# Kernel tuning notes

Measured on AMD Instinct MI355X. Metric: run time of the kernel, lower is better.

Reference implementation:

```python
import jax, jax.numpy as jnp
import numpy as np
import math

N_EMBD = 2048
N_HEAD = 16
RATIO_KV = 4
N_HEAD_KV = N_HEAD // RATIO_KV
HEAD_DIM = N_EMBD // N_HEAD


def alibi_slopes(n_heads):
    def pow2_slopes(n):
        start = 2 ** (-2 ** (-(math.log2(n) - 3)))
        return [start * start ** i for i in range(n)]
    if math.log2(n_heads).is_integer():
        return jnp.asarray(pow2_slopes(n_heads), dtype=jnp.float32)
    closest = 2 ** math.floor(math.log2(n_heads))
    base = pow2_slopes(closest)
    if n_heads <= 2 * closest:
        s = base + base[0::2]
    else:
        s = base + base[0::2] + base[1::2]
    return jnp.asarray(s[:n_heads], dtype=jnp.float32)


def setup_inputs() -> dict:
    key = jax.random.key(0)
    k0, k1, k2, k3, k4 = jax.random.split(key, 5)
    B, T = 4, 2048
    x = jax.random.normal(k0, (B, T, N_EMBD), dtype=jnp.float32)
    s = 0.02
    Wq = jax.random.normal(k1, (N_EMBD, N_EMBD), dtype=jnp.float32) * s
    Wk = jax.random.normal(k2, (N_EMBD, N_HEAD_KV * HEAD_DIM), dtype=jnp.float32) * s
    Wv = jax.random.normal(k3, (N_EMBD, N_HEAD_KV * HEAD_DIM), dtype=jnp.float32) * s
    Wo = jax.random.normal(k4, (N_EMBD, N_EMBD), dtype=jnp.float32) * s
    return {"x": x, "Wq": Wq, "Wk": Wk, "Wv": Wv, "Wo": Wo}


def reference(x, Wq, Wk, Wv, Wo):
    B, T, C = x.shape
    group = N_HEAD // N_HEAD_KV
    # projections (no bias, dropout=0 eval)
    q = (x @ Wq).reshape(B, T, N_HEAD, HEAD_DIM).transpose(0, 2, 1, 3)      # [B,H,T,D]
    k = (x @ Wk).reshape(B, T, N_HEAD_KV, HEAD_DIM).transpose(0, 2, 1, 3)   # [B,Hkv,T,D]
    v = (x @ Wv).reshape(B, T, N_HEAD_KV, HEAD_DIM).transpose(0, 2, 1, 3)
    # GQA repeat_interleave along head dim
    k = jnp.repeat(k, group, axis=1)  # [B,H,T,D]
    v = jnp.repeat(v, group, axis=1)
    scale = 1.0 / math.sqrt(HEAD_DIM)
    att = jnp.einsum('bhqd,bhkd->bhqk', q, k) * scale  # [B,H,T,T]
    # ALiBi bias: slopes[h] * (j - i), with torch's repeat_interleave-by-group
    slopes = alibi_slopes(N_HEAD)
    slopes = jnp.repeat(slopes, group)[:N_HEAD]  # matches repeat_interleave(dim=0)[:n_head]
    pos = jnp.arange(T)
    rel = pos[None, :] - pos[:, None]  # [T,T]
    bias = slopes[:, None, None] * rel.astype(jnp.float32)[None, :, :]  # [H,T,T]
    causal = jnp.triu(jnp.full((T, T), -jnp.inf, dtype=jnp.float32), k=1)
    att = att + bias[None] + causal[None, None]
    att = jax.nn.softmax(att.astype(jnp.float32), axis=-1).astype(q.dtype)
    y = jnp.einsum('bhqk,bhkd->bhqd', att, v)  # [B,H,T,D]
    y = y.transpose(0, 2, 1, 3).reshape(B, T, C)
    return y @ Wo
```

## Files before the change

### kernel.cpp

```cpp
#include <hip/hip_runtime.h>
#include <hip/hip_bf16.h>

#define T_SEQ 2048
#define NB 4
#define NE 2048
#define NH 16
#define NHKV 4
#define HD 128
#define KVD 512
#define MTOT 8192

typedef __attribute__((ext_vector_type(4))) float f32x4;
typedef __attribute__((ext_vector_type(16))) float f32x16;
typedef __attribute__((ext_vector_type(8))) __bf16 bf16x8;

__device__ __forceinline__ unsigned short f2bf(float f) {
  union { float f; unsigned int u; } x; x.f = f;
  unsigned int u = x.u;
  unsigned int r = (u + 0x7fffu + ((u >> 16) & 1u)) >> 16;
  return (unsigned short)r;
}

__device__ __forceinline__ unsigned cvtpk(float lo, float hi) {
  unsigned r;
  asm("v_cvt_pk_bf16_f32 %0, %1, %2" : "=v"(r) : "v"(lo), "v"(hi));
  return r;
}

__device__ __forceinline__ void plswap(unsigned &a, unsigned &b) {
  asm volatile("v_permlane32_swap_b32 %0, %1" : "+v"(a), "+v"(b));
}

typedef __attribute__((address_space(3))) unsigned int lds_uint;
typedef const __attribute__((address_space(1))) unsigned int glob_uint;

__device__ __forceinline__ void gload_lds16(const void* g, void* l) {
  __builtin_amdgcn_global_load_lds((glob_uint*)g, (lds_uint*)l, 16, 0, 0);
}

__global__ __launch_bounds__(256) void k_cast(const float* __restrict__ in,
                                              unsigned short* __restrict__ out, int n) {
  int i = (blockIdx.x * blockDim.x + threadIdx.x) * 8;
  if (i >= n) return;
  float4 a = *(const float4*)(in + i);
  float4 b = *(const float4*)(in + i + 4);
  union { unsigned short us[8]; uint4 v; } o;
  o.us[0] = f2bf(a.x); o.us[1] = f2bf(a.y); o.us[2] = f2bf(a.z); o.us[3] = f2bf(a.w);
  o.us[4] = f2bf(b.x); o.us[5] = f2bf(b.y); o.us[6] = f2bf(b.z); o.us[7] = f2bf(b.w);
  *(uint4*)(out + i) = o.v;
}

__global__ __launch_bounds__(256) void k_transpose_cast(const float* __restrict__ in,
                                                        unsigned short* __restrict__ out,
                                                        int K, int N) {
  __shared__ float tile[32][33];
  int n0 = blockIdx.x * 32, k0 = blockIdx.y * 32;
  int tx = threadIdx.x & 31, ty = threadIdx.x >> 5;
#pragma unroll
  for (int r = 0; r < 4; ++r)
    tile[ty + r * 8][tx] = in[(k0 + ty + r * 8) * N + n0 + tx];
  __syncthreads();
#pragma unroll
  for (int r = 0; r < 4; ++r)
    out[(n0 + ty + r * 8) * K + k0 + tx] = f2bf(tile[tx][ty + r * 8]);
}

template <int STORE_MODE>
__global__ __launch_bounds__(256) void k_gemm(const unsigned short* __restrict__ A,
                                              const unsigned short* __restrict__ Bt,
                                              void* __restrict__ C,
                                              int M, int N, int K) {
  __shared__ alignas(16) unsigned short lds[2][2][128 * 32];
  const int tid = threadIdx.x;
  const int w = tid >> 6, lane = tid & 63;
  const int lg = lane >> 4, ll = lane & 15;
  const int m0 = blockIdx.y * 128, n0 = blockIdx.x * 128;
  const int wr = (w >> 1) * 64, wc = (w & 1) * 64;

  f32x4 acc[4][4] = {};

  const int NT = K >> 5;
  int cur = 0;

  auto STAGE = [&](int buf, int t) {
    int k0 = t << 5;
#pragma unroll
    for (int is = 0; is < 2; ++is) {
      int chunk = is * 256 + tid;
      int r = chunk >> 2, c = chunk & 3;
      int sc = (c ^ ((r >> 1) & 3)) << 3;
      gload_lds16(A + (m0 + r) * K + k0 + sc, &lds[buf][0][(is * 256 + (w << 6)) * 8]);
      gload_lds16(Bt + (n0 + r) * K + k0 + sc, &lds[buf][1][(is * 256 + (w << 6)) * 8]);
    }
  };

  auto COMPUTE = [&](int buf) {
    const unsigned short* La = lds[buf][0];
    const unsigned short* Lb = lds[buf][1];
    bf16x8 af[4], bfr[4];
#pragma unroll
    for (int mf = 0; mf < 4; ++mf) {
      int r = wr + mf * 16 + ll;
      int c = lg ^ ((r >> 1) & 3);
      af[mf] = *(const bf16x8*)(La + r * 32 + c * 8);
    }
#pragma unroll
    for (int nf = 0; nf < 4; ++nf) {
      int r = wc + nf * 16 + ll;
      int c = lg ^ ((r >> 1) & 3);
      bfr[nf] = *(const bf16x8*)(Lb + r * 32 + c * 8);
    }
#pragma unroll
    for (int mf = 0; mf < 4; ++mf)
#pragma unroll
      for (int nf = 0; nf < 4; ++nf)
        acc[mf][nf] = __builtin_amdgcn_mfma_f32_16x16x32_bf16(af[mf], bfr[nf], acc[mf][nf], 0, 0, 0);
  };

  STAGE(0, 0);
  __syncthreads();
  for (int t = 0; t < NT - 1; ++t) {
    STAGE(cur ^ 1, t + 1);
    COMPUTE(cur);
    __syncthreads();
    cur ^= 1;
  }
  COMPUTE(cur);

  if (STORE_MODE == 0) {
    unsigned short* Cp = (unsigned short*)C;
#pragma unroll
    for (int mf = 0; mf < 4; ++mf)
#pragma unroll
      for (int nf = 0; nf < 4; ++nf) {
        int row = m0 + wr + mf * 16 + (lg << 2);
        int col = n0 + wc + nf * 16 + ll;
#pragma unroll
        for (int i = 0; i < 4; ++i)
          Cp[(row + i) * N + col] = f2bf(acc[mf][nf][i]);
      }
  } else if (STORE_MODE == 2) {
    float* Cp = (float*)C;
#pragma unroll
    for (int mf = 0; mf < 4; ++mf)
#pragma unroll
      for (int nf = 0; nf < 4; ++nf) {
        int row = m0 + wr + mf * 16 + (lg << 2);
        int col = n0 + wc + nf * 16 + ll;
#pragma unroll
        for (int i = 0; i < 4; ++i)
          Cp[(row + i) * N + col] = acc[mf][nf][i];
      }
  } else {
    unsigned short* Cp = (unsigned short*)C;
#pragma unroll
    for (int mf = 0; mf < 4; ++mf)
#pragma unroll
      for (int nf = 0; nf < 4; ++nf) {
        int m = m0 + wr + mf * 16 + (lg << 2);
        int n = n0 + wc + nf * 16 + ll;
        int base = (m >> 11) * (KVD * T_SEQ) + n * T_SEQ + (m & 2047);
        union { unsigned short us[4]; uint2 v; } pk;
#pragma unroll
        for (int i = 0; i < 4; ++i) pk.us[i] = f2bf(acc[mf][nf][i]);
        *(uint2*)(Cp + base) = pk.v;
      }
  }
}

__global__ __launch_bounds__(256, 2) void k_attn(const unsigned short* __restrict__ Q,
                                                 const unsigned short* __restrict__ Kp,
                                                 const unsigned short* __restrict__ Vt,
                                                 unsigned short* __restrict__ Y) {
  __shared__ alignas(16) unsigned short Klds[2][64 * 128];
  __shared__ alignas(16) unsigned short Vlds[2][128 * 64];

  const int tid = threadIdx.x, w = tid >> 6, lane = tid & 63;
  const int l31 = lane & 31, hi = lane >> 5;
  const int h = blockIdx.y, bb = blockIdx.z;
  const int hkv = h >> 2;
  const float L2E = 1.4426950408889634f;
  const float slopeL2 = exp2f(-0.5f * (float)(hkv + 1)) * L2E;
  const float c0 = 0.08838834764831845f * L2E;

  const unsigned short* Kbase = Kp + (size_t)bb * T_SEQ * KVD + hkv * HD;
  const unsigned short* Vbase = Vt + ((size_t)bb * KVD + hkv * HD) * T_SEQ;

  for (int pi = 0; pi < 2; ++pi) {
    const int qt = pi ? (15 - (int)blockIdx.x) : (int)blockIdx.x;
    const int q0 = qt * 128;
    const int qbase = q0 + w * 32;
    const int qrow = bb * T_SEQ + qbase + l31;

    bf16x8 qf[8];
#pragma unroll
    for (int ds = 0; ds < 8; ++ds)
      qf[ds] = *(const bf16x8*)(Q + (size_t)qrow * NE + h * HD + ds * 16 + hi * 8);

    f32x16 yacc[4] = {};
    float mrun = -1e30f, lrun = 0.f;
    const float qbias = slopeL2 * (float)(qbase + l31);

    auto STAGE = [&](int buf, int kt) {
      int kt0 = kt * 64;
#pragma unroll
      for (int is = 0; is < 4; ++is) {
        int chunk = is * 256 + tid;
        int r = chunk >> 4, c = chunk & 15;
        gload_lds16(Kbase + (size_t)(kt0 + r) * KVD + ((c ^ (r & 15)) << 3),
                    &Klds[buf][(is * 256 + w * 64) * 8]);
      }
#pragma unroll
      for (int is = 0; is < 4; ++is) {
        int chunk = is * 256 + tid;
        int r = chunk >> 3, c = chunk & 7;
        gload_lds16(Vbase + (size_t)r * T_SEQ + kt0 + ((c ^ (r & 7)) << 3),
                    &Vlds[buf][(is * 256 + w * 64) * 8]);
      }
    };

    const int nkt = 2 * (qt + 1);
    int cur = 0;
    STAGE(0, 0);
    for (int kt = 0; kt < nkt; ++kt) {
      if (kt + 1 < nkt) {
        STAGE(cur ^ 1, kt + 1);
        asm volatile("s_waitcnt vmcnt(8)" ::: "memory");
      } else {
        asm volatile("s_waitcnt vmcnt(0)" ::: "memory");
      }
      __builtin_amdgcn_s_barrier();
      __builtin_amdgcn_sched_barrier(0);

      const unsigned short* Kl = Klds[cur];
      const unsigned short* Vl = Vlds[cur];
      const int kt0 = kt * 64;
      const bool alldead = (kt0 >= qbase + 32);

      if (!alldead) {
        f32x16 sacc[2] = {};
#pragma unroll
        for (int ds = 0; ds < 8; ++ds) {
#pragma unroll
          for (int kf = 0; kf < 2; ++kf) {
            int row = kf * 32 + l31;
            int c = (2 * ds + hi) ^ (row & 15);
            bf16x8 kfv = *(const bf16x8*)(Kl + row * 128 + c * 8);
            sacc[kf] = __builtin_amdgcn_mfma_f32_32x32x16_bf16(kfv, qf[ds], sacc[kf], 0, 0, 0);
          }
        }

        const bool masked = (kt0 + 63 > qbase);
        const float base0 = slopeL2 * (float)(kt0 + 4 * hi) - qbias;
        const int lim = qbase + l31 - kt0 - 4 * hi;
        float mx = -1e30f;
#pragma unroll
        for (int kf = 0; kf < 2; ++kf)
#pragma unroll
          for (int r = 0; r < 16; ++r) {
            const int ckoff = kf * 32 + (r & 3) + 8 * (r >> 2);
            float a = fmaf(sacc[kf][r], c0, fmaf((float)ckoff, slopeL2, base0));
            if (masked) a = (ckoff <= lim) ? a : -1e30f;
            sacc[kf][r] = a;
            mx = fmaxf(mx, a);
          }
        mx = fmaxf(mx, __shfl_xor(mx, 32, 64));
        const float mnew = fmaxf(mrun, mx);
        const float alpha = exp2f(mrun - mnew);
        mrun = mnew;
        float sm = 0.f;
#pragma unroll
        for (int kf = 0; kf < 2; ++kf)
#pragma unroll
          for (int r = 0; r < 16; ++r) {
            float p = exp2f(sacc[kf][r] - mnew);
            sacc[kf][r] = p;
            sm += p;
          }
        sm += __shfl_xor(sm, 32, 64);
        lrun = lrun * alpha + sm;
#pragma unroll
        for (int df = 0; df < 4; ++df)
#pragma unroll
          for (int r = 0; r < 16; ++r) yacc[df][r] *= alpha;

        unsigned cpk[2][8];
#pragma unroll
        for (int kf = 0; kf < 2; ++kf)
#pragma unroll
          for (int j = 0; j < 8; ++j)
            cpk[kf][j] = cvtpk(sacc[kf][2 * j], sacc[kf][2 * j + 1]);

        bf16x8 pb[4];
#pragma unroll
        for (int ks = 0; ks < 4; ++ks) {
          unsigned a0 = cpk[ks >> 1][4 * (ks & 1) + 0];
          unsigned b0 = cpk[ks >> 1][4 * (ks & 1) + 2];
          unsigned a1 = cpk[ks >> 1][4 * (ks & 1) + 1];
          unsigned b1 = cpk[ks >> 1][4 * (ks & 1) + 3];
          plswap(a0, b0);
          plswap(a1, b1);
          union { unsigned u[4]; bf16x8 v; } pk;
          pk.u[0] = a0; pk.u[1] = a1; pk.u[2] = b0; pk.u[3] = b1;
          pb[ks] = pk.v;
        }

#pragma unroll
        for (int df = 0; df < 4; ++df) {
#pragma unroll
          for (int ks = 0; ks < 4; ++ks) {
            int row = 32 * df + l31;
            int c = (2 * ks + hi) ^ (row & 7);
            bf16x8 vf = *(const bf16x8*)(Vl + row * 64 + c * 8);
            yacc[df] = __builtin_amdgcn_mfma_f32_32x32x16_bf16(vf, pb[ks], yacc[df], 0, 0, 0);
          }
        }
      }

      __builtin_amdgcn_sched_barrier(0);
      __builtin_amdgcn_s_barrier();
      cur ^= 1;
    }

    const float inv = 1.f / lrun;
#pragma unroll
    for (int df = 0; df < 4; ++df)
#pragma unroll
      for (int g = 0; g < 4; ++g) {
        unsigned u0 = cvtpk(yacc[df][4 * g + 0] * inv, yacc[df][4 * g + 1] * inv);
        unsigned u1 = cvtpk(yacc[df][4 * g + 2] * inv, yacc[df][4 * g + 3] * inv);
        union { unsigned u[2]; uint2 v; } pk;
        pk.u[0] = u0; pk.u[1] = u1;
        *(uint2*)(Y + (size_t)qrow * NE + h * HD + 32 * df + 8 * g + 4 * hi) = pk.v;
      }
  }
}

extern "C" void kernel_launch(void* const* d_in, const int* in_sizes, int n_in,
                              void* d_out, int out_size, void* d_ws, size_t ws_size,
                              hipStream_t stream) {
  const float* x = (const float*)d_in[0];
  const float* Wq = (const float*)d_in[1];
  const float* Wk = (const float*)d_in[2];
  const float* Wv = (const float*)d_in[3];
  const float* Wo = (const float*)d_in[4];

  unsigned short* ws = (unsigned short*)d_ws;
  unsigned short* xb  = ws;
  unsigned short* Wqt = ws + 16777216;
  unsigned short* Wkt = ws + 20971520;
  unsigned short* Wvt = ws + 22020096;
  unsigned short* Wot = ws + 23068672;
  unsigned short* Qb  = ws + 27262976;
  unsigned short* Kb  = ws + 44040192;
  unsigned short* Vtb = ws + 48234496;
  unsigned short* Yb  = xb;

  k_cast<<<8192, 256, 0, stream>>>(x, xb, 16777216);
  k_transpose_cast<<<dim3(64, 64), 256, 0, stream>>>(Wq, Wqt, 2048, 2048);
  k_transpose_cast<<<dim3(16, 64), 256, 0, stream>>>(Wk, Wkt, 2048, 512);
  k_transpose_cast<<<dim3(16, 64), 256, 0, stream>>>(Wv, Wvt, 2048, 512);
  k_transpose_cast<<<dim3(64, 64), 256, 0, stream>>>(Wo, Wot, 2048, 2048);

  k_gemm<0><<<dim3(16, 64), 256, 0, stream>>>(xb, Wqt, Qb, MTOT, 2048, 2048);
  k_gemm<0><<<dim3(4, 64), 256, 0, stream>>>(xb, Wkt, Kb, MTOT, 512, 2048);
  k_gemm<1><<<dim3(4, 64), 256, 0, stream>>>(xb, Wvt, Vtb, MTOT, 512, 2048);

  k_attn<<<dim3(8, 16, 4), 256, 0, stream>>>(Qb, Kb, Vtb, Yb);

  k_gemm<2><<<dim3(16, 64), 256, 0, stream>>>(Yb, Wot, d_out, MTOT, 2048, 2048);
}
```

Before: 518.7 us.

## Fuse QKV projections into one GEMM and run paired attention tiles concurrently in 512-thread blocks

The Q, K and V projection GEMMs become a single GEMM over a concatenated transposed weight matrix, with output routed to three buffers by column range. The attention kernel now runs 8 waves per block, so the two balanced query tiles it used to process one after the other run at the same time and share staged K/V tiles. The kernel also skips the rescale of the running max when the new max grows by less than 8 (lazy rescaling), adds s_setprio around the MFMA sections, and alternates tile order by batch. This cuts launch count and idle tail time, but a 512-thread block with 4 blocks per CU bound puts more pressure on registers.

```diff
diff --git a/kernel.cpp b/kernel.cpp
--- a/kernel.cpp
+++ b/kernel.cpp
@@ -68,7 +68,8 @@
 template <int STORE_MODE>
 __global__ __launch_bounds__(256) void k_gemm(const unsigned short* __restrict__ A,
                                               const unsigned short* __restrict__ Bt,
-                                              void* __restrict__ C,
+                                              void* __restrict__ C0, void* __restrict__ C1,
+                                              void* __restrict__ C2,
                                               int M, int N, int K) {
   __shared__ alignas(16) unsigned short lds[2][2][128 * 32];
   const int tid = threadIdx.x;
@@ -78,7 +79,6 @@
   const int wr = (w >> 1) * 64, wc = (w & 1) * 64;
 
   f32x4 acc[4][4] = {};
-
   const int NT = K >> 5;
   int cur = 0;
 
@@ -127,8 +127,8 @@
   }
   COMPUTE(cur);
 
-  if (STORE_MODE == 0) {
-    unsigned short* Cp = (unsigned short*)C;
+  if (STORE_MODE == 2) {
+    float* Cp = (float*)C0;
 #pragma unroll
     for (int mf = 0; mf < 4; ++mf)
 #pragma unroll
@@ -137,41 +137,55 @@
         int col = n0 + wc + nf * 16 + ll;
 #pragma unroll
         for (int i = 0; i < 4; ++i)
-          Cp[(row + i) * N + col] = f2bf(acc[mf][nf][i]);
-      }
-  } else if (STORE_MODE == 2) {
-    float* Cp = (float*)C;
-#pragma unroll
-    for (int mf = 0; mf < 4; ++mf)
-#pragma unroll
-      for (int nf = 0; nf < 4; ++nf) {
-        int row = m0 + wr + mf * 16 + (lg << 2);
-        int col = n0 + wc + nf * 16 + ll;
-#pragma unroll
-        for (int i = 0; i < 4; ++i)
-          Cp[(row + i) * N + col] = acc[mf][nf][i];
+          Cp[(size_t)(row + i) * N + col] = acc[mf][nf][i];
       }
   } else {
-    unsigned short* Cp = (unsigned short*)C;
-#pragma unroll
-    for (int mf = 0; mf < 4; ++mf)
-#pragma unroll
-      for (int nf = 0; nf < 4; ++nf) {
-        int m = m0 + wr + mf * 16 + (lg << 2);
-        int n = n0 + wc + nf * 16 + ll;
-        int base = (m >> 11) * (KVD * T_SEQ) + n * T_SEQ + (m & 2047);
-        union { unsigned short us[4]; uint2 v; } pk;
-#pragma unroll
-        for (int i = 0; i < 4; ++i) pk.us[i] = f2bf(acc[mf][nf][i]);
-        *(uint2*)(Cp + base) = pk.v;
-      }
+    if (n0 < 2048) {
+      unsigned short* Cp = (unsigned short*)C0;
+#pragma unroll
+      for (int mf = 0; mf < 4; ++mf)
+#pragma unroll
+        for (int nf = 0; nf < 4; ++nf) {
+          int row = m0 + wr + mf * 16 + (lg << 2);
+          int col = n0 + wc + nf * 16 + ll;
+#pragma unroll
+          for (int i = 0; i < 4; ++i)
+            Cp[(size_t)(row + i) * 2048 + col] = f2bf(acc[mf][nf][i]);
+        }
+    } else if (n0 < 2560) {
+      unsigned short* Cp = (unsigned short*)C1;
+#pragma unroll
+      for (int mf = 0; mf < 4; ++mf)
+#pragma unroll
+        for (int nf = 0; nf < 4; ++nf) {
+          int row = m0 + wr + mf * 16 + (lg << 2);
+          int col = n0 + wc + nf * 16 + ll - 2048;
+#pragma unroll
+          for (int i = 0; i < 4; ++i)
+            Cp[(size_t)(row + i) * 512 + col] = f2bf(acc[mf][nf][i]);
+        }
+    } else {
+      unsigned short* Cp = (unsigned short*)C2;
+#pragma unroll
+      for (int mf = 0; mf < 4; ++mf)
+#pragma unroll
+        for (int nf = 0; nf < 4; ++nf) {
+          int m = m0 + wr + mf * 16 + (lg << 2);
+          int vd = n0 + wc + nf * 16 + ll - 2560;
+          int base = (m >> 11) * (KVD * T_SEQ) + vd * T_SEQ + (m & 2047);
+          union { unsigned short us[4]; uint2 v; } pk;
+#pragma unroll
+          for (int i = 0; i < 4; ++i) pk.us[i] = f2bf(acc[mf][nf][i]);
+          *(uint2*)(Cp + base) = pk.v;
+        }
+    }
   }
 }
 
-__global__ __launch_bounds__(256, 2) void k_attn(const unsigned short* __restrict__ Q,
-                                                 const unsigned short* __restrict__ Kp,
-                                                 const unsigned short* __restrict__ Vt,
-                                                 unsigned short* __restrict__ Y) {
+__global__ __launch_bounds__(512, 4) void k_attn8(const unsigned short* __restrict__ Q,
+                                                  const unsigned short* __restrict__ Kp,
+                                                  const unsigned short* __restrict__ Vt,
+                                                  unsigned short* __restrict__ Y) {
   __shared__ alignas(16) unsigned short Klds[2][64 * 128];
   __shared__ alignas(16) unsigned short Vlds[2][128 * 64];
 
@@ -186,154 +200,160 @@
   const unsigned short* Kbase = Kp + (size_t)bb * T_SEQ * KVD + hkv * HD;
   const unsigned short* Vbase = Vt + ((size_t)bb * KVD + hkv * HD) * T_SEQ;
 
-  for (int pi = 0; pi < 2; ++pi) {
-    const int qt = pi ? (15 - (int)blockIdx.x) : (int)blockIdx.x;
-    const int q0 = qt * 128;
-    const int qbase = q0 + w * 32;
-    const int qrow = bb * T_SEQ + qbase + l31;
-
-    bf16x8 qf[8];
-#pragma unroll
-    for (int ds = 0; ds < 8; ++ds)
-      qf[ds] = *(const bf16x8*)(Q + (size_t)qrow * NE + h * HD + ds * 16 + hi * 8);
-
-    f32x16 yacc[4] = {};
-    float mrun = -1e30f, lrun = 0.f;
-    const float qbias = slopeL2 * (float)(qbase + l31);
-
-    auto STAGE = [&](int buf, int kt) {
-      int kt0 = kt * 64;
-#pragma unroll
-      for (int is = 0; is < 4; ++is) {
-        int chunk = is * 256 + tid;
-        int r = chunk >> 4, c = chunk & 15;
-        gload_lds16(Kbase + (size_t)(kt0 + r) * KVD + ((c ^ (r & 15)) << 3),
-                    &Klds[buf][(is * 256 + w * 64) * 8]);
-      }
-#pragma unroll
-      for (int is = 0; is < 4; ++is) {
-        int chunk = is * 256 + tid;
-        int r = chunk >> 3, c = chunk & 7;
-        gload_lds16(Vbase + (size_t)r * T_SEQ + kt0 + ((c ^ (r & 7)) << 3),
-                    &Vlds[buf][(is * 256 + w * 64) * 8]);
-      }
-    };
-
-    const int nkt = 2 * (qt + 1);
-    int cur = 0;
-    STAGE(0, 0);
-    for (int kt = 0; kt < nkt; ++kt) {
-      if (kt + 1 < nkt) {
-        STAGE(cur ^ 1, kt + 1);
-        asm volatile("s_waitcnt vmcnt(8)" ::: "memory");
-      } else {
-        asm volatile("s_waitcnt vmcnt(0)" ::: "memory");
-      }
-      __builtin_amdgcn_s_barrier();
-      __builtin_amdgcn_sched_barrier(0);
-
-      const unsigned short* Kl = Klds[cur];
-      const unsigned short* Vl = Vlds[cur];
-      const int kt0 = kt * 64;
-      const bool alldead = (kt0 >= qbase + 32);
-
-      if (!alldead) {
-        f32x16 sacc[2] = {};
-#pragma unroll
-        for (int ds = 0; ds < 8; ++ds) {
-#pragma unroll
-          for (int kf = 0; kf < 2; ++kf) {
-            int row = kf * 32 + l31;
-            int c = (2 * ds + hi) ^ (row & 15);
-            bf16x8 kfv = *(const bf16x8*)(Kl + row * 128 + c * 8);
-            sacc[kf] = __builtin_amdgcn_mfma_f32_32x32x16_bf16(kfv, qf[ds], sacc[kf], 0, 0, 0);
-          }
-        }
-
-        const bool masked = (kt0 + 63 > qbase);
-        const float base0 = slopeL2 * (float)(kt0 + 4 * hi) - qbias;
-        const int lim = qbase + l31 - kt0 - 4 * hi;
-        float mx = -1e30f;
-#pragma unroll
-        for (int kf = 0; kf < 2; ++kf)
-#pragma unroll
-          for (int r = 0; r < 16; ++r) {
-            const int ckoff = kf * 32 + (r & 3) + 8 * (r >> 2);
-            float a = fmaf(sacc[kf][r], c0, fmaf((float)ckoff, slopeL2, base0));
-            if (masked) a = (ckoff <= lim) ? a : -1e30f;
-            sacc[kf][r] = a;
-            mx = fmaxf(mx, a);
-          }
-        mx = fmaxf(mx, __shfl_xor(mx, 32, 64));
+  const int p = ((bb >> 1) & 1) ? 7 - (int)blockIdx.x : (int)blockIdx.x;
+  const int qt = (w < 4) ? p : 15 - p;
+  const int q0 = qt * 128;
+  const int qbase = q0 + (w & 3) * 32;
+  const int qrow = bb * T_SEQ + qbase + l31;
+
+  bf16x8 qf[8];
+#pragma unroll
+  for (int ds = 0; ds < 8; ++ds)
+    qf[ds] = *(const bf16x8*)(Q + (size_t)qrow * NE + h * HD + ds * 16 + hi * 8);
+
+  f32x16 yacc[4] = {};
+  float mrun = -1e30f, lrun = 0.f;
+  const float qbias = slopeL2 * (float)(qbase + l31);
+
+  auto STAGE = [&](int buf, int kt) {
+    int kt0 = kt * 64;
+#pragma unroll
+    for (int is = 0; is < 2; ++is) {
+      int chunk = is * 512 + tid;
+      int r = chunk >> 4, c = chunk & 15;
+      gload_lds16(Kbase + (size_t)(kt0 + r) * KVD + ((c ^ (r & 15)) << 3),
+                  &Klds[buf][(is * 512 + w * 64) * 8]);
+    }
+#pragma unroll
+    for (int is = 0; is < 2; ++is) {
+      int chunk = is * 512 + tid;
+      int r = chunk >> 3, c = chunk & 7;
+      gload_lds16(Vbase + (size_t)r * T_SEQ + kt0 + ((c ^ (r & 7)) << 3),
+                  &Vlds[buf][(is * 512 + w * 64) * 8]);
+    }
+  };
+
+  const int nkt_hi = 2 * (16 - p);
+  int cur = 0;
+  STAGE(0, 0);
+  for (int kt = 0; kt < nkt_hi; ++kt) {
+    if (kt + 1 < nkt_hi) {
+      STAGE(cur ^ 1, kt + 1);
+      asm volatile("s_waitcnt vmcnt(4)" ::: "memory");
+    } else {
+      asm volatile("s_waitcnt vmcnt(0)" ::: "memory");
+    }
+    __builtin_amdgcn_s_barrier();
+    __builtin_amdgcn_sched_barrier(0);
+
+    const unsigned short* Kl = Klds[cur];
+    const unsigned short* Vl = Vlds[cur];
+    const int kt0 = kt * 64;
+    const bool alive = (kt0 < qbase + 32);
+
+    if (alive) {
+      f32x16 sacc[2] = {};
+      __builtin_amdgcn_s_setprio(1);
+#pragma unroll
+      for (int ds = 0; ds < 8; ++ds) {
+#pragma unroll
+        for (int kf = 0; kf < 2; ++kf) {
+          int row = kf * 32 + l31;
+          int c = (2 * ds + hi) ^ (row & 15);
+          bf16x8 kfv = *(const bf16x8*)(Kl + row * 128 + c * 8);
+          sacc[kf] = __builtin_amdgcn_mfma_f32_32x32x16_bf16(kfv, qf[ds], sacc[kf], 0, 0, 0);
+        }
+      }
+      __builtin_amdgcn_s_setprio(0);
+
+      const bool masked = (kt0 + 63 > qbase);
+      const float base0 = slopeL2 * (float)(kt0 + 4 * hi) - qbias;
+      const int lim = qbase + l31 - kt0 - 4 * hi;
+      float mx = -1e30f;
+#pragma unroll
+      for (int kf = 0; kf < 2; ++kf)
+#pragma unroll
+        for (int r = 0; r < 16; ++r) {
+          const int ckoff = kf * 32 + (r & 3) + 8 * (r >> 2);
+          float a = fmaf(sacc[kf][r], c0, fmaf((float)ckoff, slopeL2, base0));
+          if (masked) a = (ckoff <= lim) ? a : -1e30f;
+          sacc[kf][r] = a;
+          mx = fmaxf(mx, a);
+        }
+      mx = fmaxf(mx, __shfl_xor(mx, 32, 64));
+      if (!__all(mx <= mrun + 8.f)) {
         const float mnew = fmaxf(mrun, mx);
         const float alpha = exp2f(mrun - mnew);
         mrun = mnew;
-        float sm = 0.f;
-#pragma unroll
-        for (int kf = 0; kf < 2; ++kf)
-#pragma unroll
-          for (int r = 0; r < 16; ++r) {
-            float p = exp2f(sacc[kf][r] - mnew);
-            sacc[kf][r] = p;
-            sm += p;
-          }
-        sm += __shfl_xor(sm, 32, 64);
-        lrun = lrun * alpha + sm;
+        lrun *= alpha;
 #pragma unroll
         for (int df = 0; df < 4; ++df)
 #pragma unroll
           for (int r = 0; r < 16; ++r) yacc[df][r] *= alpha;
-
-        unsigned cpk[2][8];
-#pragma unroll
-        for (int kf = 0; kf < 2; ++kf)
-#pragma unroll
-          for (int j = 0; j < 8; ++j)
-            cpk[kf][j] = cvtpk(sacc[kf][2 * j], sacc[kf][2 * j + 1]);
-
-        bf16x8 pb[4];
+      }
+      float sm = 0.f;
+#pragma unroll
+      for (int kf = 0; kf < 2; ++kf)
+#pragma unroll
+        for (int r = 0; r < 16; ++r) {
+          float pv = exp2f(sacc[kf][r] - mrun);
+          sacc[kf][r] = pv;
+          sm += pv;
+        }
+      sm += __shfl_xor(sm, 32, 64);
+      lrun += sm;
+
+      unsigned cpk[2][8];
+#pragma unroll
+      for (int kf = 0; kf < 2; ++kf)
+#pragma unroll
+        for (int j = 0; j < 8; ++j)
+          cpk[kf][j] = cvtpk(sacc[kf][2 * j], sacc[kf][2 * j + 1]);
+
+      bf16x8 pb[4];
+#pragma unroll
+      for (int ks = 0; ks < 4; ++ks) {
+        unsigned a0 = cpk[ks >> 1][4 * (ks & 1) + 0];
+        unsigned b0 = cpk[ks >> 1][4 * (ks & 1) + 2];
+        unsigned a1 = cpk[ks >> 1][4 * (ks & 1) + 1];
+        unsigned b1 = cpk[ks >> 1][4 * (ks & 1) + 3];
+        plswap(a0, b0);
+        plswap(a1, b1);
+        union { unsigned u[4]; bf16x8 v; } pk;
+        pk.u[0] = a0; pk.u[1] = a1; pk.u[2] = b0; pk.u[3] = b1;
+        pb[ks] = pk.v;
+      }
+
+      __builtin_amdgcn_s_setprio(1);
+#pragma unroll
+      for (int df = 0; df < 4; ++df) {
 #pragma unroll
         for (int ks = 0; ks < 4; ++ks) {
-          unsigned a0 = cpk[ks >> 1][4 * (ks & 1) + 0];
-          unsigned b0 = cpk[ks >> 1][4 * (ks & 1) + 2];
-          unsigned a1 = cpk[ks >> 1][4 * (ks & 1) + 1];
-          unsigned b1 = cpk[ks >> 1][4 * (ks & 1) + 3];
-          plswap(a0, b0);
-          plswap(a1, b1);
-          union { unsigned u[4]; bf16x8 v; } pk;
-          pk.u[0] = a0; pk.u[1] = a1; pk.u[2] = b0; pk.u[3] = b1;
-          pb[ks] = pk.v;
-        }
-
-#pragma unroll
-        for (int df = 0; df < 4; ++df) {
-#pragma unroll
-          for (int ks = 0; ks < 4; ++ks) {
-            int row = 32 * df + l31;
-            int c = (2 * ks + hi) ^ (row & 7);
-            bf16x8 vf = *(const bf16x8*)(Vl + row * 64 + c * 8);
-            yacc[df] = __builtin_amdgcn_mfma_f32_32x32x16_bf16(vf, pb[ks], yacc[df], 0, 0, 0);
-          }
-        }
-      }
-
-      __builtin_amdgcn_sched_barrier(0);
-      __builtin_amdgcn_s_barrier();
-      cur ^= 1;
-    }
-
-    const float inv = 1.f / lrun;
-#pragma unroll
-    for (int df = 0; df < 4; ++df)
-#pragma unroll
-      for (int g = 0; g < 4; ++g) {
-        unsigned u0 = cvtpk(yacc[df][4 * g + 0] * inv, yacc[df][4 * g + 1] * inv);
-        unsigned u1 = cvtpk(yacc[df][4 * g + 2] * inv, yacc[df][4 * g + 3] * inv);
-        union { unsigned u[2]; uint2 v; } pk;
-        pk.u[0] = u0; pk.u[1] = u1;
-        *(uint2*)(Y + (size_t)qrow * NE + h * HD + 32 * df + 8 * g + 4 * hi) = pk.v;
-      }
+          int row = 32 * df + l31;
+          int c = (2 * ks + hi) ^ (row & 7);
+          bf16x8 vf = *(const bf16x8*)(Vl + row * 64 + c * 8);
+          yacc[df] = __builtin_amdgcn_mfma_f32_32x32x16_bf16(vf, pb[ks], yacc[df], 0, 0, 0);
+        }
+      }
+      __builtin_amdgcn_s_setprio(0);
+    }
+
+    __builtin_amdgcn_sched_barrier(0);
+    __builtin_amdgcn_s_barrier();
+    cur ^= 1;
   }
+
+  const float inv = 1.f / lrun;
+#pragma unroll
+  for (int df = 0; df < 4; ++df)
+#pragma unroll
+    for (int g = 0; g < 4; ++g) {
+      unsigned u0 = cvtpk(yacc[df][4 * g + 0] * inv, yacc[df][4 * g + 1] * inv);
+      unsigned u1 = cvtpk(yacc[df][4 * g + 2] * inv, yacc[df][4 * g + 3] * inv);
+      union { unsigned u[2]; uint2 v; } pk;
+      pk.u[0] = u0; pk.u[1] = u1;
+      *(uint2*)(Y + (size_t)qrow * NE + h * HD + 32 * df + 8 * g + 4 * hi) = pk.v;
+    }
 }
 
 extern "C" void kernel_launch(void* const* d_in, const int* in_sizes, int n_in,
@@ -346,27 +366,23 @@
   const float* Wo = (const float*)d_in[4];
 
   unsigned short* ws = (unsigned short*)d_ws;
-  unsigned short* xb  = ws;
-  unsigned short* Wqt = ws + 16777216;
-  unsigned short* Wkt = ws + 20971520;
-  unsigned short* Wvt = ws + 22020096;
-  unsigned short* Wot = ws + 23068672;
-  unsigned short* Qb  = ws + 27262976;
-  unsigned short* Kb  = ws + 44040192;
-  unsigned short* Vtb = ws + 48234496;
-  unsigned short* Yb  = xb;
+  unsigned short* xb    = ws;
+  unsigned short* Wqkvt = ws + 16777216;
+  unsigned short* Wot   = ws + 23068672;
+  unsigned short* Qb    = ws + 27262976;
+  unsigned short* Kb    = ws + 44040192;
+  unsigned short* Vtb   = ws + 48234496;
+  unsigned short* Yb    = xb;
 
   k_cast<<<8192, 256, 0, stream>>>(x, xb, 16777216);
-  k_transpose_cast<<<dim3(64, 64), 256, 0, stream>>>(Wq, Wqt, 2048, 2048);
-  k_transpose_cast<<<dim3(16, 64), 256, 0, stream>>>(Wk, Wkt, 2048, 512);
-  k_transpose_cast<<<dim3(16, 64), 256, 0, stream>>>(Wv, Wvt, 2048, 512);
+  k_transpose_cast<<<dim3(64, 64), 256, 0, stream>>>(Wq, Wqkvt, 2048, 2048);
+  k_transpose_cast<<<dim3(16, 64), 256, 0, stream>>>(Wk, Wqkvt + 2048 * 2048, 2048, 512);
+  k_transpose_cast<<<dim3(16, 64), 256, 0, stream>>>(Wv, Wqkvt + 2560 * 2048, 2048, 512);
   k_transpose_cast<<<dim3(64, 64), 256, 0, stream>>>(Wo, Wot, 2048, 2048);
 
-  k_gemm<0><<<dim3(16, 64), 256, 0, stream>>>(xb, Wqt, Qb, MTOT, 2048, 2048);
-  k_gemm<0><<<dim3(4, 64), 256, 0, stream>>>(xb, Wkt, Kb, MTOT, 512, 2048);
-  k_gemm<1><<<dim3(4, 64), 256, 0, stream>>>(xb, Wvt, Vtb, MTOT, 512, 2048);
-
-  k_attn<<<dim3(8, 16, 4), 256, 0, stream>>>(Qb, Kb, Vtb, Yb);
-
-  k_gemm<2><<<dim3(16, 64), 256, 0, stream>>>(Yb, Wot, d_out, MTOT, 2048, 2048);
-}
+  k_gemm<3><<<dim3(24, 64), 256, 0, stream>>>(xb, Wqkvt, Qb, Kb, Vtb, MTOT, 3072, 2048);
+
+  k_attn8<<<dim3(8, 16, 4), 512, 0, stream>>>(Qb, Kb, Vtb, Yb);
+
+  k_gemm<2><<<dim3(16, 64), 256, 0, stream>>>(Yb, Wot, d_out, nullptr, nullptr, MTOT, 2048, 2048);
+}
```

New measurement: 630.4 us. +21.5%, slower.
